# Optimization experiments

Measured on AMD Instinct MI355X. Metric: run time of the kernel, lower is better.

Reference implementation:

```python
import jax, jax.numpy as jnp
import numpy as np

HEAD_NUM = 16

def setup_inputs() -> dict:
    key = jax.random.key(0)
    k1, k2 = jax.random.split(key)
    bs, seq, d = 2, 2048, 1024
    embeddings = jax.random.normal(k1, (bs, seq, d), dtype=jnp.float32)
    W = jax.random.normal(k2, (d, 3 * d), dtype=jnp.float32) * (1.0 / np.sqrt(d))
    b = jnp.zeros((3 * d,), dtype=jnp.float32)
    return {"embeddings": embeddings, "W": W, "b": b}

def reference(embeddings, W, b):
    bs, seq, d = embeddings.shape
    h = HEAD_NUM
    qkv = embeddings @ W + b                      # [b, s, 3d]
    q, k, v = jnp.split(qkv, 3, axis=-1)          # each [b, s, d]
    hd = d // h
    # Faithful to source: reshape to (bs, seq, head_dim, heads) then permute
    def split_heads(x, head_dim):
        return x.reshape(bs, seq, head_dim, h).transpose(0, 3, 1, 2)  # [b, h, s, hd]
    mq = split_heads(q, hd)
    mk = split_heads(k, hd)
    mv = split_heads(v, hd)
    scale = jnp.sqrt(jnp.asarray(hd, dtype=mq.dtype))
    scores = jnp.einsum('bhqd,bhkd->bhqk', mq, mk) / scale  # [b, h, s, s]
    attn = jax.nn.softmax(scores, axis=-1)
    out = jnp.einsum('bhqk,bhkv->bhqv', attn, mv)            # [b, h, s, hd]
    return out.transpose(0, 2, 1, 3).reshape(bs, seq, -1)    # [b, s, d]
```

## Files before the change

### kernel.cpp

```cpp
#include <hip/hip_runtime.h>
#include <stdint.h>

typedef unsigned short u16;
typedef unsigned int u32;
typedef unsigned int u32x2 __attribute__((ext_vector_type(2)));
typedef float f32x4 __attribute__((ext_vector_type(4)));
typedef __bf16 bf16x8 __attribute__((ext_vector_type(8)));

#define BS 2
#define SEQ 2048
#define DIM 1024
#define NW3 3072
#define NH 16
#define HD 64

#define MFMA_BF16(a, b, c) __builtin_amdgcn_mfma_f32_16x16x32_bf16((a), (b), (c), 0, 0, 0)

#define GLL16(g, l)                                                                \
  __builtin_amdgcn_global_load_lds(                                                \
      (__attribute__((address_space(1))) void*)(void*)(uintptr_t)(g),              \
      (__attribute__((address_space(3))) void*)(l), 16, 0, 0)

__device__ __forceinline__ float fexp2(float x) {
#if defined(__has_builtin)
#if __has_builtin(__builtin_amdgcn_exp2f)
  return __builtin_amdgcn_exp2f(x);
#else
  return exp2f(x);
#endif
#else
  return exp2f(x);
#endif
}

__device__ __forceinline__ u16 f2bf(float x) {
  __bf16 h = (__bf16)x;
  return __builtin_bit_cast(u16, h);
}

#define CSC 0.18033688011112042f

#if defined(__has_builtin)
#if __has_builtin(__builtin_amdgcn_permlane32_swap) && \
    __has_builtin(__builtin_amdgcn_permlane16_swap)
#define HAVE_PLSWAP 1
#endif
#endif

__device__ __forceinline__ uint4 p_transform(u32 pk00, u32 pk01, u32 pk10, u32 pk11,
                                             int sl0, int sl1, bool hi) {
#ifdef HAVE_PLSWAP
  u32x2 s0 = __builtin_amdgcn_permlane32_swap(pk00, pk10, false, false);
  u32x2 s1 = __builtin_amdgcn_permlane32_swap(pk01, pk11, false, false);
  u32x2 t0 = __builtin_amdgcn_permlane16_swap(s0[0], s0[1], false, false);
  u32x2 t1 = __builtin_amdgcn_permlane16_swap(s1[0], s1[1], false, false);
  uint4 wv;
  wv.x = t0[0]; wv.y = t1[0]; wv.z = t0[1]; wv.w = t1[1];
  return wv;
#else
  u32 a0 = __shfl(pk00, sl0), a1 = __shfl(pk01, sl0);
  u32 a2 = __shfl(pk00, sl1), a3 = __shfl(pk01, sl1);
  u32 b0 = __shfl(pk10, sl0), b1 = __shfl(pk11, sl0);
  u32 b2 = __shfl(pk10, sl1), b3 = __shfl(pk11, sl1);
  uint4 wv;
  wv.x = hi ? b0 : a0; wv.y = hi ? b1 : a1;
  wv.z = hi ? b2 : a2; wv.w = hi ? b3 : a3;
  return wv;
#endif
}

__global__ __launch_bounds__(256) void conv_kernel(const float* __restrict__ A,
                                                   u16* __restrict__ O,
                                                   const float* __restrict__ W,
                                                   u16* __restrict__ Wt) {
  if (blockIdx.x < 4096) {
    int i = (blockIdx.x * 256 + threadIdx.x) * 4;
    float4 v = *(const float4*)(A + i);
    union { u16 u[4]; ushort4 v4; } p;
    p.u[0] = f2bf(v.x); p.u[1] = f2bf(v.y); p.u[2] = f2bf(v.z); p.u[3] = f2bf(v.w);
    *(ushort4*)(O + i) = p.v4;
  } else {
    __shared__ __align__(16) u16 lt[64][68];
    int b2 = blockIdx.x - 4096;
    int ktile = b2 / 48, ntile = b2 - ktile * 48;
    int k0 = ktile * 64, n0 = ntile * 64;
    int rowb = threadIdx.x >> 4, c4 = (threadIdx.x & 15) * 4;
#pragma unroll
    for (int rr = 0; rr < 4; ++rr) {
      int row = rowb + rr * 16;
      float4 v = *(const float4*)(W + (size_t)(k0 + row) * NW3 + n0 + c4);
      union { u16 u[4]; uint2 d; } pk;
      pk.u[0] = f2bf(v.x); pk.u[1] = f2bf(v.y); pk.u[2] = f2bf(v.z); pk.u[3] = f2bf(v.w);
      *(uint2*)&lt[row][c4] = pk.d;
    }
    __syncthreads();
    int j = threadIdx.x >> 2, seg = threadIdx.x & 3;
    int n = n0 + j;
    int h = n & 15, hd = (n & 1023) >> 4;
    int np = (n & ~1023) + h * 64 + hd;
    union { u16 u[16]; uint4 q[2]; } o;
#pragma unroll
    for (int idx = 0; idx < 16; ++idx) o.u[idx] = lt[seg * 16 + idx][j];
    u16* dst = Wt + (size_t)np * DIM + k0 + seg * 16;
    *(uint4*)(dst) = o.q[0];
    *(uint4*)(dst + 8) = o.q[1];
  }
}

#define GSTAGE(ADST, BDST, KT)                                                 \
  {                                                                            \
    const int koff = (KT) * 64;                                \
    _Pragma("unroll") for (int r = 0; r < 2; ++r) {                            \
      int l = r * 256 + t;                            \
      int row = l >> 2, pos = l & 3;                                           \
      int kc = pos ^ (row & 3);                                                \
      GLL16(Abase + row * 2048 + koff + kc * 16, (char*)(ADST) + l * 16);      \
      GLL16(Bbase + row * 2048 + koff + kc * 16, (char*)(BDST) + l * 16);      \
    }                                                                          \
  }

#define GCOMPUTE(AT, BT)                                                       \
  {                                                                            \
    bf16x8 af[4], bfr[4];                                                      \
    _Pragma("unroll") for (int mt = 0; mt < 4; ++mt) {                         \
      int row = wm + mt * 16 + c;                                              \
      int kc = quad ^ (row & 3);                                               \
      af[mt] = *(const bf16x8*)((const char*)(AT) + row * 64 + kc * 16);       \
    }                                                                          \
    _Pragma("unroll") for (int nt = 0; nt < 4; ++nt) {                         \
      int row = wn + nt * 16 + c;                                              \
      int kc = quad ^ (row & 3);                                               \
      bfr[nt] = *(const bf16x8*)((const char*)(BT) + row * 64 + kc * 16);      \
    }                                                                          \
    _Pragma("unroll") for (int mt = 0; mt < 4; ++mt)                           \
      _Pragma("unroll") for (int nt = 0; nt < 4; ++nt)                         \
        acc[mt][nt] = MFMA_BF16(af[mt], bfr[nt], acc[mt][nt]);                 \
  }

__global__ __launch_bounds__(256) void gemm_qkv_kernel(
    const u16* __restrict__ Ab, const u16* __restrict__ Bt, const float* __restrict__ bias,
    u16* __restrict__ Q, u16* __restrict__ K, u16* __restrict__ Vt) {
  __shared__ __align__(16) u16 Aa[128 * 32];
  __shared__ __align__(16) u16 Ab2[128 * 32];
  __shared__ __align__(16) u16 Ba[128 * 32];
  __shared__ __align__(16) u16 Bb2[128 * 32];
  const int t = threadIdx.x;
  const int lane = t & 63, wave = t >> 6;
  const int c = lane & 15, quad = lane >> 4;
  const int tm = blockIdx.x / 24, tn = blockIdx.x - tm * 24;
  const int wm = (wave >> 1) * 64, wn = (wave & 1) * 64;

  const char* Abase = (const char*)(Ab + (size_t)tm * 128 * DIM);
  const char* Bbase = (const char*)(Bt + (size_t)tn * 128 * DIM);

  f32x4 z = {0.f, 0.f, 0.f, 0.f};
  f32x4 acc[4][4];
#pragma unroll
  for (int i = 0; i < 4; ++i)
#pragma unroll
    for (int j = 0; j < 4; ++j) acc[i][j] = z;

  GSTAGE(Aa, Ba, 0);
  __syncthreads();
  for (int kt = 0; kt < 32; kt += 2) {
    GSTAGE(Ab2, Bb2, kt + 1);
    GCOMPUTE(Aa, Ba);
    __syncthreads();
    if (kt + 2 < 32) GSTAGE(Aa, Ba, kt + 2);
    GCOMPUTE(Ab2, Bb2);
    __syncthreads();
  }

#pragma unroll
  for (int nt = 0; nt < 4; ++nt) {
    int np = tn * 128 + wn + nt * 16 + c;
    int which = np >> 10;
    int rem = np & 1023;
    int h = rem >> 6, hd = rem & 63;
    float bv = bias[(np & ~1023) + hd * 16 + h];
    float sc = (which == 0) ? CSC : 1.0f;
    float bvs = bv * sc;
#pragma unroll
    for (int mt = 0; mt < 4; ++mt) {
      int mbase = tm * 128 + wm + mt * 16 + quad * 4;
      int bI = mbase >> 11;
      int s0 = mbase & 2047;
      if (which == 2) {
        union { u16 u[4]; uint2 v; } p;
#pragma unroll
        for (int r = 0; r < 4; ++r) p.u[r] = f2bf(acc[mt][nt][r] + bv);
        *(uint2*)(Vt + ((size_t)(bI * NH + h) * HD + hd) * SEQ + s0) = p.v;
      } else {
        u16* dst = (which == 0) ? Q : K;
#pragma unroll
        for (int r = 0; r < 4; ++r)
          dst[((size_t)(bI * NH + h) * SEQ + (s0 + r)) * HD + hd] =
              f2bf(acc[mt][nt][r] * sc + bvs);
      }
    }
  }
}

#define STAGE_KV(KDST, VDST, KTILE)                                            \
  {                                                                            \
    const char* Ktb = Kb + (size_t)(KTILE) * 8192;        \
    const char* Vtb = Vb + (size_t)(KTILE) * 128;         \
    _Pragma("unroll") for (int r = 0; r < 2; ++r) {                            \
      int l = r * 256 + t;                                                     \
      int row = l >> 3, pos = l & 7;                                           \
      int kc = pos ^ (row & 7);                                                \
      GLL16(Ktb + row * 128 + kc * 16, (char*)(KDST) + l * 16);                \
      GLL16(Vtb + row * 4096 + kc * 16, (char*)(VDST) + l * 16);               \
    }                                                                          \
  }

#define COMPUTE_TILE(KT, VT)                                                   \
  {                                                                            \
    f32x4 sT[2][2]; \
    sT[0][0] = z; sT[0][1] = z; sT[1][0] = z; sT[1][1] = z;                    \
    __builtin_amdgcn_s_setprio(1);                                             \
    _Pragma("unroll") for (int mt2 = 0; mt2 < 2; ++mt2) {                      \
      _Pragma("unroll") for (int ks = 0; ks < 2; ++ks) {                       \
        int row = ws * 32 + mt2 * 16 + c;                                      \
        int kc = (ks * 4 + quad) ^ (row & 7);                                  \
        bf16x8 kf = *(const bf16x8*)((const char*)(KT) + row * 128 + kc * 16); \
        sT[mt2][0] = MFMA_BF16(kf, qf[0][ks], sT[mt2][0]);                     \
        sT[mt2][1] = MFMA_BF16(kf, qf[1][ks], sT[mt2][1]);                     \
      }                                                                        \
    }                                                                          \
    __builtin_amdgcn_s_setprio(0);                                             \
    bf16x8 pf[2];                                                              \
    _Pragma("unroll") for (int nt = 0; nt < 2; ++nt) {                         \
      u32 pk[2][2];                                                            \
      _Pragma("unroll") for (int mt2 = 0; mt2 < 2; ++mt2) {                    \
        float p0 = fexp2(sT[mt2][nt][0]);                                      \
        float p1 = fexp2(sT[mt2][nt][1]);                                      \
        float p2 = fexp2(sT[mt2][nt][2]);                                      \
        float p3 = fexp2(sT[mt2][nt][3]);                                      \
        pk[mt2][0] = (u32)f2bf(p0) | ((u32)f2bf(p1) << 16);                    \
        pk[mt2][1] = (u32)f2bf(p2) | ((u32)f2bf(p3) << 16);                    \
      }                                                                        \
      uint4 wv = p_transform(pk[0][0], pk[0][1], pk[1][0], pk[1][1],           \
                             sl0, sl1, hi);                                    \
      pf[nt] = __builtin_bit_cast(bf16x8, wv);                                 \
    }                                                                          \
    __builtin_amdgcn_s_setprio(1);                                             \
    _Pragma("unroll") for (int mt = 0; mt < 4; ++mt) {                         \
      int row = mt * 16 + c;                                                   \
      int kc = vq ^ (row & 7);                                                 \
      bf16x8 vf = *(const bf16x8*)((const char*)(VT) + row * 128 + kc * 16);   \
      accO[mt][0] = MFMA_BF16(vf, pf[0], accO[mt][0]);                         \
      accO[mt][1] = MFMA_BF16(vf, pf[1], accO[mt][1]);                         \
    }                                                                          \
    acc_l[0] = MFMA_BF16(ones, pf[0], acc_l[0]);   \
    acc_l[1] = MFMA_BF16(ones, pf[1], acc_l[1]);                               \
    __builtin_amdgcn_s_setprio(0);                                             \
  }

__global__ __launch_bounds__(256, 4) void attn_kernel(
    const u16* __restrict__ Q, const u16* __restrict__ K,
    const u16* __restrict__ Vt, float* __restrict__ Out) {
  __shared__ __align__(16) u16 Ka[64 * 64];
  __shared__ __align__(16) u16 Kb2[64 * 64];
  __shared__ __align__(16) u16 Va[64 * 64];
  __shared__ __align__(16) u16 Vb2[64 * 64];
  const int t = threadIdx.x;
  const int lane = t & 63, wave = t >> 6;
  const int c = lane & 15, quad = lane >> 4;
  const int wq = wave & 1, ws = wave >> 1;
  const int p = blockIdx.x;
  const int xcd = p & 7, slot = p >> 3;
  const int bh = xcd + ((slot >> 5) << 3);
  const int qt = slot & 31;
  const int h = bh & 15, b = bh >> 4;

  const u16* Qb = Q + ((size_t)bh * SEQ + qt * 64) * HD;
  const char* Kb = (const char*)(K + (size_t)bh * SEQ * HD);
  const char* Vb = (const char*)(Vt + (size_t)bh * HD * SEQ);

#pragma unroll
  for (int r = 0; r < 2; ++r) {
    int l = r * 256 + t;
    int row = l >> 3, pos = l & 7;
    int kc = pos ^ (row & 7);
    GLL16((const char*)Qb + row * 128 + kc * 16, (char*)Ka + l * 16);
  }
  __syncthreads();
  bf16x8 qf[2][2];
#pragma unroll
  for (int nt = 0; nt < 2; ++nt)
#pragma unroll
    for (int ks = 0; ks < 2; ++ks) {
      int row = wq * 32 + nt * 16 + c;
      int kc = (ks * 4 + quad) ^ (row & 7);
      qf[nt][ks] = *(const bf16x8*)((const char*)Ka + row * 128 + kc * 16);
    }
  __syncthreads();

  f32x4 z = {0.f, 0.f, 0.f, 0.f};
  f32x4 accO[4][2];
#pragma unroll
  for (int i = 0; i < 4; ++i) { accO[i][0] = z; accO[i][1] = z; }
  f32x4 acc_l[2] = {z, z};
  const uint4 onesw = {0x3F803F80u, 0x3F803F80u, 0x3F803F80u, 0x3F803F80u};
  const bf16x8 ones = __builtin_bit_cast(bf16x8, onesw);

  const int sl0 = c + 16 * ((quad & 1) * 2);
  const int sl1 = sl0 + 16;
  const bool hi = quad >= 2;
  const int vq = ws * 4 + quad;

  STAGE_KV(Ka, Va, 0);
  __syncthreads();

  for (int kt = 0; kt < 32; kt += 2) {
    STAGE_KV(Kb2, Vb2, kt + 1);
    COMPUTE_TILE(Ka, Va);
    __syncthreads();
    if (kt + 2 < 32) STAGE_KV(Ka, Va, kt + 2);
    COMPUTE_TILE(Kb2, Vb2);
    __syncthreads();
  }

  float sm[2];
  sm[0] = acc_l[0][0];
  sm[1] = acc_l[1][0];
  if (ws == 1) {
    float* fb = (float*)(wq ? (void*)Kb2 : (void*)Ka);
#pragma unroll
    for (int mt = 0; mt < 4; ++mt)
#pragma unroll
      for (int nt = 0; nt < 2; ++nt)
        *(f32x4*)(fb + (mt * 2 + nt) * 256 + lane * 4) = accO[mt][nt];
    float* lb = (float*)Va + wq * 128;
    lb[lane * 2] = sm[0];
    lb[lane * 2 + 1] = sm[1];
  }
  __syncthreads();
  if (ws == 0) {
    const float* fb = (const float*)(wq ? (void*)Kb2 : (void*)Ka);
#pragma unroll
    for (int mt = 0; mt < 4; ++mt)
#pragma unroll
      for (int nt = 0; nt < 2; ++nt)
        accO[mt][nt] += *(const f32x4*)(fb + (mt * 2 + nt) * 256 + lane * 4);
    const float* lb = (const float*)Va + wq * 128;
    float inv0 = 1.f / (sm[0] + lb[lane * 2]);
    float inv1 = 1.f / (sm[1] + lb[lane * 2 + 1]);
    int s0 = qt * 64 + wq * 32 + c;
#pragma unroll
    for (int mt = 0; mt < 4; ++mt) {
#pragma unroll
      for (int nt = 0; nt < 2; ++nt) {
        float inv = nt ? inv1 : inv0;
        float4 o;
        o.x = accO[mt][nt][0] * inv;
        o.y = accO[mt][nt][1] * inv;
        o.z = accO[mt][nt][2] * inv;
        o.w = accO[mt][nt][3] * inv;
        size_t off = ((size_t)(b * SEQ + s0 + nt * 16)) * DIM + h * HD + mt * 16 + quad * 4;
        *(float4*)(Out + off) = o;
      }
    }
  }
}

extern "C" void kernel_launch(void* const* d_in, const int* in_sizes, int n_in,
                              void* d_out, int out_size, void* d_ws, size_t ws_size,
                              hipStream_t stream) {
  (void)in_sizes; (void)n_in; (void)out_size; (void)ws_size;
  const float* emb = (const float*)d_in[0];
  const float* W = (const float*)d_in[1];
  const float* bias = (const float*)d_in[2];
  float* out = (float*)d_out;
  char* ws = (char*)d_ws;
  u16* Ab = (u16*)ws;
  u16* Wt = (u16*)(ws + 8388608);
  u16* Qd = (u16*)(ws + 14680064);
  u16* Kd = (u16*)(ws + 23068672);
  u16* Vd = (u16*)(ws + 31457280);

  conv_kernel<<<4864, 256, 0, stream>>>(emb, Ab, W, Wt);
  gemm_qkv_kernel<<<768, 256, 0, stream>>>(Ab, Wt, bias, Qd, Kd, Vd);
  attn_kernel<<<1024, 256, 0, stream>>>(Qd, Kd, Vd, out);
}
```

Before: 162.6 us.

## Load K/V fragments directly from global memory instead of staging through LDS

Removes the double-buffered LDS staging of K and V tiles, which used global_load_lds and barriers, and has each wave read its MFMA operand fragments straight from global memory into registers. The loop is unrolled by two, and LDS is kept only for the final cross-wave reduction buffer. This drops per-tile __syncthreads and LDS traffic, but each K/V element is now fetched by both query-half waves, which doubles global/L2 reads. Latency hiding now depends on the compiler scheduling loads ahead and on occupancy.

Result: slower. 229.2 us (+41.0%).

```diff
diff --git a/kernel.cpp b/kernel.cpp
--- a/kernel.cpp
+++ b/kernel.cpp
@@ -201,31 +201,21 @@
   }
 }
 
-#define STAGE_KV(KDST, VDST, KTILE)                                            \
+#define TILE(KT)                                                               \
   {                                                                            \
-    const char* Ktb = Kb + (size_t)(KTILE) * 8192;        \
-    const char* Vtb = Vb + (size_t)(KTILE) * 128;         \
-    _Pragma("unroll") for (int r = 0; r < 2; ++r) {                            \
-      int l = r * 256 + t;                                                     \
-      int row = l >> 3, pos = l & 7;                                           \
-      int kc = pos ^ (row & 7);                                                \
-      GLL16(Ktb + row * 128 + kc * 16, (char*)(KDST) + l * 16);                \
-      GLL16(Vtb + row * 4096 + kc * 16, (char*)(VDST) + l * 16);               \
-    }                                                                          \
-  }
-
-#define COMPUTE_TILE(KT, VT)                                                   \
-  {                                                                            \
-    f32x4 sT[2][2]; \
+    bf16x8 kf[2][2], vf[4];                                                    \
+    _Pragma("unroll") for (int mt2 = 0; mt2 < 2; ++mt2)                        \
+      _Pragma("unroll") for (int ks = 0; ks < 2; ++ks)                         \
+        kf[mt2][ks] = *(const bf16x8*)(Kbp + ((KT) * 64 + ws * 32 + mt2 * 16 + c) * 128 + (ks * 4 + quad) * 16); \
+    _Pragma("unroll") for (int mt = 0; mt < 4; ++mt)                           \
+      vf[mt] = *(const bf16x8*)(Vbp + (mt * 16 + c) * 4096 + (KT) * 128 + ws * 64 + quad * 16); \
+    f32x4 sT[2][2];                                                            \
     sT[0][0] = z; sT[0][1] = z; sT[1][0] = z; sT[1][1] = z;                    \
     __builtin_amdgcn_s_setprio(1);                                             \
     _Pragma("unroll") for (int mt2 = 0; mt2 < 2; ++mt2) {                      \
       _Pragma("unroll") for (int ks = 0; ks < 2; ++ks) {                       \
-        int row = ws * 32 + mt2 * 16 + c;                                      \
-        int kc = (ks * 4 + quad) ^ (row & 7);                                  \
-        bf16x8 kf = *(const bf16x8*)((const char*)(KT) + row * 128 + kc * 16); \
-        sT[mt2][0] = MFMA_BF16(kf, qf[0][ks], sT[mt2][0]);                     \
-        sT[mt2][1] = MFMA_BF16(kf, qf[1][ks], sT[mt2][1]);                     \
+        sT[mt2][0] = MFMA_BF16(kf[mt2][ks], qf[0][ks], sT[mt2][0]);            \
+        sT[mt2][1] = MFMA_BF16(kf[mt2][ks], qf[1][ks], sT[mt2][1]);            \
       }                                                                        \
     }                                                                          \
     __builtin_amdgcn_s_setprio(0);                                             \
@@ -246,13 +236,10 @@
     }                                                                          \
     __builtin_amdgcn_s_setprio(1);                                             \
     _Pragma("unroll") for (int mt = 0; mt < 4; ++mt) {                         \
-      int row = mt * 16 + c;                                                   \
-      int kc = vq ^ (row & 7);                                                 \
-      bf16x8 vf = *(const bf16x8*)((const char*)(VT) + row * 128 + kc * 16);   \
-      accO[mt][0] = MFMA_BF16(vf, pf[0], accO[mt][0]);                         \
-      accO[mt][1] = MFMA_BF16(vf, pf[1], accO[mt][1]);                         \
-    }                                                                          \
-    acc_l[0] = MFMA_BF16(ones, pf[0], acc_l[0]);   \
+      accO[mt][0] = MFMA_BF16(vf[mt], pf[0], accO[mt][0]);                     \
+      accO[mt][1] = MFMA_BF16(vf[mt], pf[1], accO[mt][1]);                     \
+    }                                                                          \
+    acc_l[0] = MFMA_BF16(ones, pf[0], acc_l[0]);                               \
     acc_l[1] = MFMA_BF16(ones, pf[1], acc_l[1]);                               \
     __builtin_amdgcn_s_setprio(0);                                             \
   }
@@ -260,10 +247,7 @@
 __global__ __launch_bounds__(256, 4) void attn_kernel(
     const u16* __restrict__ Q, const u16* __restrict__ K,
     const u16* __restrict__ Vt, float* __restrict__ Out) {
-  __shared__ __align__(16) u16 Ka[64 * 64];
-  __shared__ __align__(16) u16 Kb2[64 * 64];
-  __shared__ __align__(16) u16 Va[64 * 64];
-  __shared__ __align__(16) u16 Vb2[64 * 64];
+  __shared__ __align__(16) float red[4352];
   const int t = threadIdx.x;
   const int lane = t & 63, wave = t >> 6;
   const int c = lane & 15, quad = lane >> 4;
@@ -274,28 +258,16 @@
   const int qt = slot & 31;
   const int h = bh & 15, b = bh >> 4;
 
-  const u16* Qb = Q + ((size_t)bh * SEQ + qt * 64) * HD;
-  const char* Kb = (const char*)(K + (size_t)bh * SEQ * HD);
-  const char* Vb = (const char*)(Vt + (size_t)bh * HD * SEQ);
-
-#pragma unroll
-  for (int r = 0; r < 2; ++r) {
-    int l = r * 256 + t;
-    int row = l >> 3, pos = l & 7;
-    int kc = pos ^ (row & 7);
-    GLL16((const char*)Qb + row * 128 + kc * 16, (char*)Ka + l * 16);
-  }
-  __syncthreads();
+  const char* Qbp = (const char*)(Q + ((size_t)bh * SEQ + qt * 64) * HD);
+  const char* Kbp = (const char*)(K + (size_t)bh * SEQ * HD);
+  const char* Vbp = (const char*)(Vt + (size_t)bh * HD * SEQ);
+
   bf16x8 qf[2][2];
 #pragma unroll
   for (int nt = 0; nt < 2; ++nt)
 #pragma unroll
-    for (int ks = 0; ks < 2; ++ks) {
-      int row = wq * 32 + nt * 16 + c;
-      int kc = (ks * 4 + quad) ^ (row & 7);
-      qf[nt][ks] = *(const bf16x8*)((const char*)Ka + row * 128 + kc * 16);
-    }
-  __syncthreads();
+    for (int ks = 0; ks < 2; ++ks)
+      qf[nt][ks] = *(const bf16x8*)(Qbp + (wq * 32 + nt * 16 + c) * 128 + (ks * 4 + quad) * 16);
 
   f32x4 z = {0.f, 0.f, 0.f, 0.f};
   f32x4 accO[4][2];
@@ -308,43 +280,35 @@
   const int sl0 = c + 16 * ((quad & 1) * 2);
   const int sl1 = sl0 + 16;
   const bool hi = quad >= 2;
-  const int vq = ws * 4 + quad;
-
-  STAGE_KV(Ka, Va, 0);
-  __syncthreads();
-
-  for (int kt = 0; kt < 32; kt += 2) {
-    STAGE_KV(Kb2, Vb2, kt + 1);
-    COMPUTE_TILE(Ka, Va);
-    __syncthreads();
-    if (kt + 2 < 32) STAGE_KV(Ka, Va, kt + 2);
-    COMPUTE_TILE(Kb2, Vb2);
-    __syncthreads();
+
+#pragma unroll 2
+  for (int kt = 0; kt < 32; ++kt) {
+    TILE(kt);
   }
 
   float sm[2];
   sm[0] = acc_l[0][0];
   sm[1] = acc_l[1][0];
   if (ws == 1) {
-    float* fb = (float*)(wq ? (void*)Kb2 : (void*)Ka);
+    float* fb = red + wq * 2048;
 #pragma unroll
     for (int mt = 0; mt < 4; ++mt)
 #pragma unroll
       for (int nt = 0; nt < 2; ++nt)
         *(f32x4*)(fb + (mt * 2 + nt) * 256 + lane * 4) = accO[mt][nt];
-    float* lb = (float*)Va + wq * 128;
+    float* lb = red + 4096 + wq * 128;
     lb[lane * 2] = sm[0];
     lb[lane * 2 + 1] = sm[1];
   }
   __syncthreads();
   if (ws == 0) {
-    const float* fb = (const float*)(wq ? (void*)Kb2 : (void*)Ka);
+    const float* fb = red + wq * 2048;
 #pragma unroll
     for (int mt = 0; mt < 4; ++mt)
 #pragma unroll
       for (int nt = 0; nt < 2; ++nt)
         accO[mt][nt] += *(const f32x4*)(fb + (mt * 2 + nt) * 256 + lane * 4);
-    const float* lb = (const float*)Va + wq * 128;
+    const float* lb = red + 4096 + wq * 128;
     float inv0 = 1.f / (sm[0] + lb[lane * 2]);
     float inv1 = 1.f / (sm[1] + lb[lane * 2 + 1]);
     int s0 = qt * 64 + wq * 32 + c;
```
